# Optimization experiments

Hardware: AMD Instinct MI355X
Metric: run time of the kernel (lower is better)

The kernel has to match this reference:

```python
import jax, jax.numpy as jnp
import numpy as np

P_DIM, M_DIM = 512, 768
PROJ, HID, NCLS = 512, 256, 2
EPS = 1e-5


def _bn_eval(x, g, b):
    # BatchNorm1d in eval mode with fresh buffers: running_mean=0, running_var=1
    return x / jnp.sqrt(1.0 + EPS) * g + b


def setup_inputs() -> dict:
    key = jax.random.key(0)
    ks = jax.random.split(key, 8)
    x = jax.random.normal(ks[0], (256, P_DIM + M_DIM), dtype=jnp.float32)
    W1 = jax.random.normal(ks[1], (PROJ, P_DIM * M_DIM), dtype=jnp.float32) * 0.002
    b1 = jnp.zeros((PROJ,), jnp.float32)
    ln_g = jnp.ones((PROJ,), jnp.float32)
    ln_b = jnp.zeros((PROJ,), jnp.float32)
    W2 = jax.random.normal(ks[2], (HID, PROJ), dtype=jnp.float32) * 0.04
    b2 = jnp.zeros((HID,), jnp.float32)
    bn1_g = jnp.ones((HID,), jnp.float32)
    bn1_b = jnp.zeros((HID,), jnp.float32)
    W3 = jax.random.normal(ks[3], (HID // 2, HID), dtype=jnp.float32) * 0.06
    b3 = jnp.zeros((HID // 2,), jnp.float32)
    bn2_g = jnp.ones((HID // 2,), jnp.float32)
    bn2_b = jnp.zeros((HID // 2,), jnp.float32)
    W4 = jax.random.normal(ks[4], (NCLS, HID // 2), dtype=jnp.float32) * 0.09
    b4 = jnp.zeros((NCLS,), jnp.float32)
    return dict(x=x, W1=W1, b1=b1, ln_g=ln_g, ln_b=ln_b, W2=W2, b2=b2,
                bn1_g=bn1_g, bn1_b=bn1_b, W3=W3, b3=b3,
                bn2_g=bn2_g, bn2_b=bn2_b, W4=W4, b4=b4)


def reference(x, W1, b1, ln_g, ln_b, W2, b2, bn1_g, bn1_b, W3, b3, bn2_g, bn2_b, W4, b4):
    p = x[:, :P_DIM]                     # [B, P]
    m = x[:, P_DIM:P_DIM + M_DIM]        # [B, M]
    # kron[b, i*M + j] = p[b,i]*m[b,j]; Linear(kron_flat) fused into one contraction
    W1r = W1.reshape(PROJ, P_DIM, M_DIM)
    fused = jnp.einsum('bp,bm,kpm->bk', p, m, W1r) + b1   # [B, PROJ]
    # LayerNorm + ReLU (dropout is identity in eval)
    mu = jnp.mean(fused, axis=-1, keepdims=True)
    var = jnp.var(fused, axis=-1, keepdims=True)
    h = (fused - mu) / jnp.sqrt(var + EPS) * ln_g + ln_b
    h = jax.nn.relu(h)
    # classifier MLP with BatchNorm1d (eval-mode buffers)
    h = jax.nn.relu(_bn_eval(h @ W2.T + b2, bn1_g, bn1_b))
    h = jax.nn.relu(_bn_eval(h @ W3.T + b3, bn2_g, bn2_b))
    logits = h @ W4.T + b4               # [B, NCLS]
    return logits
```

## Files before the change

### kernel.cpp

```cpp
#include <hip/hip_runtime.h>
#include <hip/hip_bf16.h>

typedef __attribute__((ext_vector_type(4))) float f32x4;
typedef __attribute__((ext_vector_type(16))) float f32x16;
typedef __attribute__((ext_vector_type(8))) short short8;
typedef unsigned short ushort_t;

#define BATCH 256
#define PDIM 512
#define MDIM 768
#define XCOLS 1280
#define PROJ 512
#define HID 256
#define KTOT (PDIM * MDIM)

#define BN 64
#define NT 8
#define PSPLIT 64
#define PI_PER 8
#define NJW 12
#define NSTEPS 96

__device__ __forceinline__ ushort_t f2bf(float f) {
  __hip_bfloat16 h = __float2bfloat16(f);
  return __builtin_bit_cast(ushort_t, h);
}

__global__ void prep_kernel(const float* __restrict__ x, float* __restrict__ pT,
                            ushort_t* __restrict__ mF) {
  int tid = blockIdx.x * blockDim.x + threadIdx.x;
  int nth = gridDim.x * blockDim.x;
  for (int i = tid; i < PDIM * BATCH; i += nth) {
    int pi = i >> 8, b = i & 255;
    pT[i] = x[b * XCOLS + pi];
  }
  for (int c = tid; c < NJW * 8 * 4 * 64; c += nth) {
    int lane = c & 63;
    int ks = (c >> 6) & 3;
    int mf = (c >> 8) & 7;
    int jw = c >> 11;
    int row = mf * 32 + (lane & 31);
    int k0 = jw * 64 + ks * 16 + ((lane >> 5) << 3);
    const float* src = x + row * XCOLS + PDIM + k0;
    f32x4 v0 = *(const f32x4*)src;
    f32x4 v1 = *(const f32x4*)(src + 4);
    short8 o;
#pragma unroll
    for (int i = 0; i < 4; ++i) {
      o[i] = (short)f2bf(v0[i]);
      o[i + 4] = (short)f2bf(v1[i]);
    }
    ((short8*)mF)[c] = o;
  }
}

__global__ __launch_bounds__(512, 4)
void einsum_kernel(const float* __restrict__ W1, const ushort_t* __restrict__ mF,
                   const float* __restrict__ pT, float* __restrict__ outp,
                   int atomic_mode) {
  __shared__ ushort_t Af[16384];
  __shared__ ushort_t Bf[2][4096];
  __shared__ float pl[PI_PER * BATCH];

  const int ntile = blockIdx.x & 7;
  const int ps    = blockIdx.x >> 3;
  const int pi0   = ps * PI_PER;
  const int n0    = ntile * BN;
  const int t     = threadIdx.x;
  const int lane  = t & 63;
  const int wave  = t >> 6;
  const int wm    = wave & 3;
  const int wn    = wave >> 2;

  ((f32x4*)pl)[t] = ((const f32x4*)(pT + pi0 * BATCH))[t];

  const int sn = t >> 3, sq = t & 7;
  const int bofs = (((sn >> 5) * 4 + (sq >> 1)) * 64 + (sn & 31) + ((sq & 1) << 5)) * 8;
  const float* wbase = W1 + (size_t)(n0 + sn) * KTOT + sq * 8;

  const int aidx0 = wm * 512 + lane;
  const int aidx1 = aidx0 + 256;
  const int bidx  = wn * 256 + lane;

  f32x16 fa0, fa1;
#pragma unroll
  for (int i = 0; i < 16; ++i) { fa0[i] = 0.f; fa1[i] = 0.f; }
  f32x16 zz;
#pragma unroll
  for (int i = 0; i < 16; ++i) zz[i] = 0.f;

  f32x4 c0, c1, nv0, nv1;
  {
    const float* wp = wbase + (size_t)pi0 * MDIM;
    c0 = *(const f32x4*)wp;
    c1 = *(const f32x4*)(wp + 4);
  }

  const short8* AfV = (const short8*)Af;

  for (int s = 0; s < NSTEPS; ++s) {
    const int pil = s & 7;
    const int jw  = s >> 3;
    const bool boundary = (pil == 0);

    if (!boundary) {
      const int s1 = s + 1;
      const float* wp = wbase + (size_t)(pi0 + (s1 & 7)) * MDIM + (s1 >> 3) * 64;
      nv0 = *(const f32x4*)wp;
      nv1 = *(const f32x4*)(wp + 4);
    }

    {
      short8 bs;
#pragma unroll
      for (int i = 0; i < 4; ++i) {
        bs[i]     = (short)f2bf(c0[i]);
        bs[i + 4] = (short)f2bf(c1[i]);
      }
      *(short8*)(&Bf[s & 1][bofs]) = bs;
    }
    asm volatile("s_waitcnt lgkmcnt(0)" ::: "memory");
    __builtin_amdgcn_s_barrier();
    asm volatile("" ::: "memory");

    if (boundary) {
      const short8* srcA = (const short8*)(mF + jw * 16384);
      short8 a0 = srcA[t * 4 + 0];
      short8 a1 = srcA[t * 4 + 1];
      short8 a2 = srcA[t * 4 + 2];
      short8 a3 = srcA[t * 4 + 3];
      {
        const int s1 = s + 1;
        const float* wp = wbase + (size_t)(pi0 + (s1 & 7)) * MDIM + (s1 >> 3) * 64;
        nv0 = *(const f32x4*)wp;
        nv1 = *(const f32x4*)(wp + 4);
      }
      ((short8*)Af)[t * 4 + 0] = a0;
      ((short8*)Af)[t * 4 + 1] = a1;
      ((short8*)Af)[t * 4 + 2] = a2;
      ((short8*)Af)[t * 4 + 3] = a3;
      asm volatile("s_waitcnt lgkmcnt(0)" ::: "memory");
      __builtin_amdgcn_s_barrier();
      asm volatile("" ::: "memory");
    }

    const short8* BfV = (const short8*)Bf[s & 1];
    f32x16 ap0, ap1;
    {
      short8 av0 = AfV[aidx0];
      short8 av1 = AfV[aidx1];
      short8 bv  = BfV[bidx];
      ap0 = __builtin_amdgcn_mfma_f32_32x32x16_bf16(av0, bv, zz, 0, 0, 0);
      ap1 = __builtin_amdgcn_mfma_f32_32x32x16_bf16(av1, bv, zz, 0, 0, 0);
    }
#pragma unroll
    for (int ks = 1; ks < 4; ++ks) {
      short8 av0 = AfV[aidx0 + ks * 64];
      short8 av1 = AfV[aidx1 + ks * 64];
      short8 bv  = BfV[bidx + ks * 64];
      ap0 = __builtin_amdgcn_mfma_f32_32x32x16_bf16(av0, bv, ap0, 0, 0, 0);
      ap1 = __builtin_amdgcn_mfma_f32_32x32x16_bf16(av1, bv, ap1, 0, 0, 0);
    }

    {
      const float* prow = pl + pil * BATCH;
      const int rb = wm * 64 + ((lane >> 5) << 2);
#pragma unroll
      for (int q = 0; q < 4; ++q) {
        f32x4 p0 = *(const f32x4*)(prow + rb + 8 * q);
        f32x4 p1 = *(const f32x4*)(prow + rb + 32 + 8 * q);
#pragma unroll
        for (int j = 0; j < 4; ++j) {
          fa0[q * 4 + j] += p0[j] * ap0[q * 4 + j];
          fa1[q * 4 + j] += p1[j] * ap1[q * 4 + j];
        }
      }
    }

    c0 = nv0; c1 = nv1;
  }

  const int col   = n0 + wn * 32 + (lane & 31);
  const int rbase = wm * 64 + ((lane >> 5) << 2);
  if (atomic_mode) {
#pragma unroll
    for (int r = 0; r < 16; ++r) {
      int row = rbase + (r & 3) + ((r >> 2) << 3);
      atomicAdd(&outp[(size_t)row * PROJ + col], fa0[r]);
      atomicAdd(&outp[(size_t)(row + 32) * PROJ + col], fa1[r]);
    }
  } else {
    float* dst = outp + (size_t)ps * BATCH * PROJ;
#pragma unroll
    for (int r = 0; r < 16; ++r) {
      int row = rbase + (r & 3) + ((r >> 2) << 3);
      dst[(size_t)row * PROJ + col] = fa0[r];
      dst[(size_t)(row + 32) * PROJ + col] = fa1[r];
    }
  }
}

__global__ __launch_bounds__(256)
void mlp_kernel(const float* __restrict__ part, int nps,
                const float* __restrict__ b1, const float* __restrict__ lng,
                const float* __restrict__ lnb, const float* __restrict__ W2,
                const float* __restrict__ b2, const float* __restrict__ g1,
                const float* __restrict__ bb1, const float* __restrict__ W3,
                const float* __restrict__ b3, const float* __restrict__ g2,
                const float* __restrict__ bb2, const float* __restrict__ W4,
                const float* __restrict__ b4, float* __restrict__ out) {
  __shared__ float h1[PROJ];
  __shared__ float h2[HID];
  __shared__ float h3[HID / 2];
  __shared__ float red[16];
  const int b = blockIdx.x, t = threadIdx.x;

  float f0 = 0.f, f1 = 0.f;
  const float* p0 = part + (size_t)b * PROJ + t;
#pragma unroll 4
  for (int s = 0; s < nps; ++s) {
    f0 += p0[0];
    f1 += p0[256];
    p0 += (size_t)BATCH * PROJ;
  }
  f0 += b1[t];
  f1 += b1[t + 256];

  float sum = f0 + f1, ss = f0 * f0 + f1 * f1;
#pragma unroll
  for (int o = 32; o > 0; o >>= 1) {
    sum += __shfl_xor(sum, o);
    ss  += __shfl_xor(ss, o);
  }
  const int wv = t >> 6, ln = t & 63;
  if (ln == 0) { red[wv] = sum; red[8 + wv] = ss; }
  __syncthreads();
  sum = red[0] + red[1] + red[2] + red[3];
  ss  = red[8] + red[9] + red[10] + red[11];
  float mu   = sum * (1.f / 512.f);
  float var  = ss * (1.f / 512.f) - mu * mu;
  float rstd = rsqrtf(var + 1e-5f);
  h1[t]       = fmaxf(0.f, (f0 - mu) * rstd * lng[t] + lnb[t]);
  h1[t + 256] = fmaxf(0.f, (f1 - mu) * rstd * lng[t + 256] + lnb[t + 256]);
  __syncthreads();

  const float bninv = rsqrtf(1.f + 1e-5f);
  {
    const f32x4* wr = (const f32x4*)(W2 + (size_t)t * PROJ);
    const f32x4* hv = (const f32x4*)h1;
    float a = 0.f;
#pragma unroll 4
    for (int i = 0; i < PROJ / 4; ++i) {
      f32x4 w = wr[i], h = hv[i];
      a += w[0] * h[0] + w[1] * h[1] + w[2] * h[2] + w[3] * h[3];
    }
    h2[t] = fmaxf(0.f, (a + b2[t]) * bninv * g1[t] + bb1[t]);
  }
  __syncthreads();
  if (t < 128) {
    const f32x4* wr = (const f32x4*)(W3 + (size_t)t * HID);
    const f32x4* hv = (const f32x4*)h2;
    float a = 0.f;
#pragma unroll 4
    for (int i = 0; i < HID / 4; ++i) {
      f32x4 w = wr[i], h = hv[i];
      a += w[0] * h[0] + w[1] * h[1] + w[2] * h[2] + w[3] * h[3];
    }
    h3[t] = fmaxf(0.f, (a + b3[t]) * bninv * g2[t] + bb2[t]);
  }
  __syncthreads();
  if (t < 2) {
    const float* wr = W4 + t * 128;
    float a = 0.f;
#pragma unroll 4
    for (int i = 0; i < 128; ++i) a += wr[i] * h3[i];
    out[b * 2 + t] = a + b4[t];
  }
}

extern "C" void kernel_launch(void* const* d_in, const int* in_sizes, int n_in,
                              void* d_out, int out_size, void* d_ws, size_t ws_size,
                              hipStream_t stream) {
  const float* x   = (const float*)d_in[0];
  const float* W1  = (const float*)d_in[1];
  const float* b1  = (const float*)d_in[2];
  const float* lng = (const float*)d_in[3];
  const float* lnb = (const float*)d_in[4];
  const float* W2  = (const float*)d_in[5];
  const float* b2  = (const float*)d_in[6];
  const float* g1  = (const float*)d_in[7];
  const float* bb1 = (const float*)d_in[8];
  const float* W3  = (const float*)d_in[9];
  const float* b3  = (const float*)d_in[10];
  const float* g2  = (const float*)d_in[11];
  const float* bb2 = (const float*)d_in[12];
  const float* W4  = (const float*)d_in[13];
  const float* b4  = (const float*)d_in[14];
  float* out = (float*)d_out;

  char* ws = (char*)d_ws;
  float* pT    = (float*)ws;
  ushort_t* mF = (ushort_t*)(ws + 524288);
  float* big   = (float*)(ws + 1048576);

  size_t need = 1048576 + (size_t)PSPLIT * BATCH * PROJ * 4;
  bool partial = ws_size >= need;

  hipLaunchKernelGGL(prep_kernel, dim3(512), dim3(256), 0, stream, x, pT, mF);
  if (partial) {
    hipLaunchKernelGGL(einsum_kernel, dim3(NT * PSPLIT), dim3(512), 0, stream,
                       W1, mF, pT, big, 0);
    hipLaunchKernelGGL(mlp_kernel, dim3(BATCH), dim3(256), 0, stream, big, PSPLIT,
                       b1, lng, lnb, W2, b2, g1, bb1, W3, b3, g2, bb2, W4, b4, out);
  } else {
    hipMemsetAsync(big, 0, (size_t)BATCH * PROJ * 4, stream);
    hipLaunchKernelGGL(einsum_kernel, dim3(NT * PSPLIT), dim3(512), 0, stream,
                       W1, mF, pT, big, 1);
    hipLaunchKernelGGL(mlp_kernel, dim3(BATCH), dim3(256), 0, stream, big, 1,
                       b1, lng, lnb, W2, b2, g1, bb1, W3, b3, g2, bb2, W4, b4, out);
  }
}
```

Measured before the change: 234.0 us.

## Fold p scaling into the bf16 A operand and accumulate directly in MFMA

```diff
diff --git a/kernel.cpp b/kernel.cpp
--- a/kernel.cpp
+++ b/kernel.cpp
@@ -24,6 +24,11 @@
 __device__ __forceinline__ ushort_t f2bf(float f) {
   __hip_bfloat16 h = __float2bfloat16(f);
   return __builtin_bit_cast(ushort_t, h);
+}
+__device__ __forceinline__ float bf2f(ushort_t u) {
+  union { unsigned int i; float f; } c;
+  c.i = ((unsigned int)u) << 16;
+  return c.f;
 }
 
 __global__ void prep_kernel(const float* __restrict__ x, float* __restrict__ pT,
@@ -59,7 +64,7 @@
                    const float* __restrict__ pT, float* __restrict__ outp,
                    int atomic_mode) {
   __shared__ ushort_t Af[16384];
-  __shared__ ushort_t Bf[2][4096];
+  __shared__ ushort_t Bf[4096];
   __shared__ float pl[PI_PER * BATCH];
 
   const int ntile = blockIdx.x & 7;
@@ -74,9 +79,16 @@
 
   ((f32x4*)pl)[t] = ((const f32x4*)(pT + pi0 * BATCH))[t];
 
-  const int sn = t >> 3, sq = t & 7;
-  const int bofs = (((sn >> 5) * 4 + (sq >> 1)) * 64 + (sn & 31) + ((sq & 1) << 5)) * 8;
-  const float* wbase = W1 + (size_t)(n0 + sn) * KTOT + sq * 8;
+  const int sn = t >> 3, q = t & 7;
+  const float* wbase = W1 + (size_t)(n0 + sn) * KTOT + (size_t)pi0 * MDIM + q * 8;
+  const int bwo = (((sn >> 5) * 4 + (q >> 1)) * 64 + ((q & 1) << 5) + (sn & 31)) * 8;
+
+  int arow[4];
+#pragma unroll
+  for (int i = 0; i < 4; ++i) {
+    int c = t + 512 * i;
+    arow[i] = (c >> 8) * 32 + (c & 31);
+  }
 
   const int aidx0 = wm * 512 + lane;
   const int aidx1 = aidx0 + 256;
@@ -85,99 +97,85 @@
   f32x16 fa0, fa1;
 #pragma unroll
   for (int i = 0; i < 16; ++i) { fa0[i] = 0.f; fa1[i] = 0.f; }
-  f32x16 zz;
-#pragma unroll
-  for (int i = 0; i < 16; ++i) zz[i] = 0.f;
-
-  f32x4 c0, c1, nv0, nv1;
+
+  f32x4 wv0 = *(const f32x4*)(wbase);
+  f32x4 wv1 = *(const f32x4*)(wbase + 4);
+  short8 ac0, ac1, ac2, ac3;
   {
-    const float* wp = wbase + (size_t)pi0 * MDIM;
-    c0 = *(const f32x4*)wp;
-    c1 = *(const f32x4*)(wp + 4);
-  }
+    const short8* src = (const short8*)mF;
+    ac0 = src[t];
+    ac1 = src[t + 512];
+    ac2 = src[t + 1024];
+    ac3 = src[t + 1536];
+  }
+  asm volatile("s_waitcnt lgkmcnt(0)" ::: "memory");
+  __builtin_amdgcn_s_barrier();
+  asm volatile("" ::: "memory");
 
   const short8* AfV = (const short8*)Af;
+  const short8* BfV = (const short8*)Bf;
+  int jwc = 0, pilc = 0;
 
   for (int s = 0; s < NSTEPS; ++s) {
-    const int pil = s & 7;
-    const int jw  = s >> 3;
-    const bool boundary = (pil == 0);
-
-    if (!boundary) {
-      const int s1 = s + 1;
-      const float* wp = wbase + (size_t)(pi0 + (s1 & 7)) * MDIM + (s1 >> 3) * 64;
+    f32x4 nv0, nv1;
+    {
+      const int s1 = (s + 1 < NSTEPS) ? s + 1 : 0;
+      const float* wp = wbase + s1 * 64;
       nv0 = *(const f32x4*)wp;
       nv1 = *(const f32x4*)(wp + 4);
     }
-
     {
       short8 bs;
 #pragma unroll
       for (int i = 0; i < 4; ++i) {
-        bs[i]     = (short)f2bf(c0[i]);
-        bs[i + 4] = (short)f2bf(c1[i]);
+        bs[i]     = (short)f2bf(wv0[i]);
+        bs[i + 4] = (short)f2bf(wv1[i]);
       }
-      *(short8*)(&Bf[s & 1][bofs]) = bs;
+      *(short8*)&Bf[bwo] = bs;
+    }
+    {
+      const float* prow = pl + pilc * BATCH;
+      float p0 = prow[arow[0]], p1 = prow[arow[1]];
+      float p2 = prow[arow[2]], p3 = prow[arow[3]];
+      short8 o0, o1, o2, o3;
+#pragma unroll
+      for (int e = 0; e < 8; ++e) {
+        o0[e] = (short)f2bf(p0 * bf2f((ushort_t)ac0[e]));
+        o1[e] = (short)f2bf(p1 * bf2f((ushort_t)ac1[e]));
+        o2[e] = (short)f2bf(p2 * bf2f((ushort_t)ac2[e]));
+        o3[e] = (short)f2bf(p3 * bf2f((ushort_t)ac3[e]));
+      }
+      ((short8*)Af)[t]        = o0;
+      ((short8*)Af)[t + 512]  = o1;
+      ((short8*)Af)[t + 1024] = o2;
+      ((short8*)Af)[t + 1536] = o3;
     }
     asm volatile("s_waitcnt lgkmcnt(0)" ::: "memory");
     __builtin_amdgcn_s_barrier();
     asm volatile("" ::: "memory");
 
-    if (boundary) {
-      const short8* srcA = (const short8*)(mF + jw * 16384);
-      short8 a0 = srcA[t * 4 + 0];
-      short8 a1 = srcA[t * 4 + 1];
-      short8 a2 = srcA[t * 4 + 2];
-      short8 a3 = srcA[t * 4 + 3];
-      {
-        const int s1 = s + 1;
-        const float* wp = wbase + (size_t)(pi0 + (s1 & 7)) * MDIM + (s1 >> 3) * 64;
-        nv0 = *(const f32x4*)wp;
-        nv1 = *(const f32x4*)(wp + 4);
-      }
-      ((short8*)Af)[t * 4 + 0] = a0;
-      ((short8*)Af)[t * 4 + 1] = a1;
-      ((short8*)Af)[t * 4 + 2] = a2;
-      ((short8*)Af)[t * 4 + 3] = a3;
-      asm volatile("s_waitcnt lgkmcnt(0)" ::: "memory");
-      __builtin_amdgcn_s_barrier();
-      asm volatile("" ::: "memory");
-    }
-
-    const short8* BfV = (const short8*)Bf[s & 1];
-    f32x16 ap0, ap1;
     {
-      short8 av0 = AfV[aidx0];
-      short8 av1 = AfV[aidx1];
-      short8 bv  = BfV[bidx];
-      ap0 = __builtin_amdgcn_mfma_f32_32x32x16_bf16(av0, bv, zz, 0, 0, 0);
-      ap1 = __builtin_amdgcn_mfma_f32_32x32x16_bf16(av1, bv, zz, 0, 0, 0);
-    }
-#pragma unroll
-    for (int ks = 1; ks < 4; ++ks) {
+      const int jn = (jwc + 1 == NJW) ? 0 : jwc + 1;
+      const short8* src = (const short8*)mF + jn * 2048;
+      ac0 = src[t];
+      ac1 = src[t + 512];
+      ac2 = src[t + 1024];
+      ac3 = src[t + 1536];
+    }
+#pragma unroll
+    for (int ks = 0; ks < 4; ++ks) {
       short8 av0 = AfV[aidx0 + ks * 64];
       short8 av1 = AfV[aidx1 + ks * 64];
       short8 bv  = BfV[bidx + ks * 64];
-      ap0 = __builtin_amdgcn_mfma_f32_32x32x16_bf16(av0, bv, ap0, 0, 0, 0);
-      ap1 = __builtin_amdgcn_mfma_f32_32x32x16_bf16(av1, bv, ap1, 0, 0, 0);
-    }
-
-    {
-      const float* prow = pl + pil * BATCH;
-      const int rb = wm * 64 + ((lane >> 5) << 2);
-#pragma unroll
-      for (int q = 0; q < 4; ++q) {
-        f32x4 p0 = *(const f32x4*)(prow + rb + 8 * q);
-        f32x4 p1 = *(const f32x4*)(prow + rb + 32 + 8 * q);
-#pragma unroll
-        for (int j = 0; j < 4; ++j) {
-          fa0[q * 4 + j] += p0[j] * ap0[q * 4 + j];
-          fa1[q * 4 + j] += p1[j] * ap1[q * 4 + j];
-        }
-      }
-    }
-
-    c0 = nv0; c1 = nv1;
+      fa0 = __builtin_amdgcn_mfma_f32_32x32x16_bf16(av0, bv, fa0, 0, 0, 0);
+      fa1 = __builtin_amdgcn_mfma_f32_32x32x16_bf16(av1, bv, fa1, 0, 0, 0);
+    }
+    asm volatile("s_waitcnt lgkmcnt(0)" ::: "memory");
+    __builtin_amdgcn_s_barrier();
+    asm volatile("" ::: "memory");
+
+    wv0 = nv0; wv1 = nv1;
+    if (++jwc == NJW) { jwc = 0; ++pilc; }
   }
 
   const int col   = n0 + wn * 32 + (lane & 31);
```

Result: slower. 251.9 us (+7.7%).
